# Kernel tuning notes

Hardware: AMD Instinct MI355X
Metric: run time of the kernel (lower is better)

Reference implementation:

```python
import jax, jax.numpy as jnp
import numpy as np

THETA_BASE = 10000.0

def rope(x, pos_offset=0):
    # x: (B, S, D), D even. Rotates interleaved (even, odd) dim pairs.
    B, S, D = x.shape
    pos = jnp.arange(pos_offset, pos_offset + S, dtype=jnp.float32)[:, None]  # (S,1)
    p = jnp.arange(D // 2, dtype=jnp.float32)  # p-1 in source, 0-indexed here
    theta = pos * (THETA_BASE ** (-2.0 * p / D))  # (S, D//2)
    sin_t, cos_t = jnp.sin(theta), jnp.cos(theta)
    x1, x2 = x[..., 0::2], x[..., 1::2]
    r1 = x1 * cos_t - x2 * sin_t
    r2 = x1 * sin_t + x2 * cos_t
    return jnp.stack((r1, r2), axis=-1).reshape(B, S, D)

def setup_inputs() -> dict:
    key = jax.random.key(0)
    k1, k2, k3, k4 = jax.random.split(key, 4)
    B, S, E, Dh = 4, 4096, 2048, 128
    return {
        "x": jax.random.normal(k1, (B, S, E), dtype=jnp.float32),
        "W_Q": jax.random.normal(k2, (E, Dh), dtype=jnp.float32) / np.sqrt(E),
        "W_K": jax.random.normal(k3, (E, Dh), dtype=jnp.float32) / np.sqrt(E),
        "W_V": jax.random.normal(k4, (E, Dh), dtype=jnp.float32) / np.sqrt(E),
    }

def reference(x, W_Q, W_K, W_V):
    d_h = W_Q.shape[1]
    past_len = 0  # kv_cache is None (prefill)
    Q = rope(x @ W_Q, pos_offset=past_len)  # NOTE: source ropes Q and V, not K
    K = x @ W_K
    V = rope(x @ W_V, pos_offset=past_len)
    scores = jnp.einsum('bqd,bkd->bqk', Q, K) / jnp.sqrt(jnp.float32(d_h))
    S_q, S_total = scores.shape[-2], scores.shape[-1]
    i = jnp.arange(S_q)[:, None] + past_len
    j = jnp.arange(S_total)[None, :]
    causal = j <= i  # (S_q, S_total) bool
    masked = jnp.where(causal[None, :, :], scores, jnp.float32(-jnp.inf))
    attn = jax.nn.softmax(masked, axis=-1)
    return jnp.einsum('bqk,bkd->bqd', attn, V)
```

## Files before the change

### kernel.cpp

```cpp
#include <hip/hip_runtime.h>
#include <hip/hip_bf16.h>
#include <stdint.h>

#define S_LEN 4096
#define E_DIM 2048
#define DH    128

typedef __bf16 bf16_t;
typedef bf16_t bf16x8 __attribute__((ext_vector_type(8)));
typedef float  f32x4  __attribute__((ext_vector_type(4)));

__device__ __forceinline__ unsigned short f2bf(float f) {
  union { float f; uint32_t u; } v; v.f = f;
  uint32_t u = v.u;
  uint32_t r = (u + 0x7fffu + ((u >> 16) & 1u)) >> 16;
  return (unsigned short)r;
}

__device__ __forceinline__ bf16x8 ld_bf16x8(const unsigned short* p) {
  return *(const bf16x8*)p;
}

__device__ __forceinline__ f32x4 mfma16(bf16x8 a, bf16x8 b, f32x4 c) {
  return __builtin_amdgcn_mfma_f32_16x16x32_bf16(a, b, c, 0, 0, 0);
}

__device__ __forceinline__ void gload16(const void* gsrc, void* ldst) {
  __builtin_amdgcn_global_load_lds(
      (const __attribute__((address_space(1))) uint32_t*)gsrc,
      (__attribute__((address_space(3))) uint32_t*)ldst, 16, 0, 0);
}

__global__ __launch_bounds__(256) void prep_kernel(
    const float* __restrict__ WQ, const float* __restrict__ WK,
    const float* __restrict__ WV,
    float2* __restrict__ trig, unsigned short* __restrict__ Wt)
{
  const int bx  = blockIdx.x;
  const int tid = threadIdx.x;
  if (bx < 1024) {
    const int idx = bx * 256 + tid;
    const int pos = idx >> 6, p = idx & 63;
    const float freq = powf(10000.0f, -(float)p / 64.0f);
    float sv, cv;
    sincosf((float)pos * freq, &sv, &cv);
    trig[idx] = make_float2(cv, sv);
    return;
  }
  __shared__ float lds[64][65];
  const int t   = bx - 1024;
  const int z   = t >> 6;
  const int rem = t & 63;
  const int k0  = (rem >> 1) * 64;
  const int n0  = (rem & 1) * 64;
  const float* W = (z == 0) ? WQ : ((z == 1) ? WK : WV);
  #pragma unroll
  for (int pass = 0; pass < 4; pass++) {
    const int r  = pass * 16 + (tid >> 4);
    const int c4 = (tid & 15) * 4;
    float4 v = *(const float4*)(W + (size_t)(k0 + r) * 128 + n0 + c4);
    lds[c4 + 0][r] = v.x; lds[c4 + 1][r] = v.y;
    lds[c4 + 2][r] = v.z; lds[c4 + 3][r] = v.w;
  }
  __syncthreads();
  #pragma unroll
  for (int pass = 0; pass < 4; pass++) {
    const int n  = pass * 16 + (tid >> 4);
    const int k4 = (tid & 15) * 4;
    ushort4 pk;
    pk.x = f2bf(lds[n][k4 + 0]); pk.y = f2bf(lds[n][k4 + 1]);
    pk.z = f2bf(lds[n][k4 + 2]); pk.w = f2bf(lds[n][k4 + 3]);
    *(ushort4*)(Wt + (size_t)(z * 128 + n0 + n) * E_DIM + k0 + k4) = pk;
  }
}

__global__ __launch_bounds__(256, 4) void proj_kernel(
    const float* __restrict__ x, const unsigned short* __restrict__ Wt,
    const float2* __restrict__ trig,
    unsigned short* __restrict__ Qb, unsigned short* __restrict__ Kb,
    unsigned short* __restrict__ Vt)
{
  __shared__ __align__(16) uint8_t Abuf[2][64 * 128];
  __shared__ __align__(16) uint8_t Bbuf[2][96 * 128];

  const int tid  = threadIdx.x;
  const int lane = tid & 63, w2 = tid >> 6;
  const int wr = w2 & 1, wc = w2 >> 1;
  const int col = lane & 15, kg = lane >> 4;

  const int m0 = blockIdx.x * 64;
  const int p  = blockIdx.y;

  f32x4 acc[2][3];
  #pragma unroll
  for (int i = 0; i < 2; i++)
    #pragma unroll
    for (int j = 0; j < 3; j++) acc[i][j] = (f32x4){0.f, 0.f, 0.f, 0.f};

  const int a_r = lane >> 4;
  const int a_c = (lane & 15) * 4;
  const int b_r  = lane >> 3;
  const int b_cb = (lane & 7) * 16;

  float4 R0[4], R1[4];

  #define ALOAD(R, K0)                                                        \
    do {                                                                      \
      _Pragma("unroll")                                                       \
      for (int j = 0; j < 4; j++) {                                           \
        const int row = w2 * 16 + j * 4 + a_r;                                \
        R[j] = *(const float4*)(x + (size_t)(m0 + row) * E_DIM + (K0) + a_c); \
      }                                                                       \
    } while (0)

  #define BSTAGE(K0, BUF)                                                     \
    do {                                                                      \
      _Pragma("unroll")                                                       \
      for (int c = 0; c < 3; c++) {                                           \
        const int seg = w2 * 3 + c;                                           \
        const int row = seg * 8 + b_r;                                        \
        const int src = b_cb ^ ((row & 7) << 4);                              \
        gload16((const char*)Wt + ((size_t)(p * 96 + row) * E_DIM + (K0)) * 2 + src,\
                &Bbuf[BUF][seg * 1024]);                                      \
      }                                                                       \
    } while (0)

  #define AWRITE(R, BUF)                                                      \
    do {                                                                      \
      _Pragma("unroll")                                                       \
      for (int j = 0; j < 4; j++) {                                           \
        const int row = w2 * 16 + j * 4 + a_r;                                \
        ushort4 h;                                                            \
        h.x = f2bf(R[j].x); h.y = f2bf(R[j].y);                               \
        h.z = f2bf(R[j].z); h.w = f2bf(R[j].w);                               \
        const int dst = (a_c * 2) ^ ((row & 7) << 4);                         \
        *(ushort4*)(&Abuf[BUF][row * 128 + dst]) = h;                         \
      }                                                                       \
    } while (0)

  #define COMP(BUF)                                                           \
    do {                                                                      \
      _Pragma("unroll")                                                       \
      for (int kk = 0; kk < 2; kk++) {                                        \
        bf16x8 af[2];                                                         \
        _Pragma("unroll")                                                     \
        for (int i = 0; i < 2; i++) {                                         \
          const int row = wr * 32 + i * 16 + col;                             \
          af[i] = *(const bf16x8*)(&Abuf[BUF][row * 128 +                     \
                   ((kk * 64 + kg * 16) ^ ((row & 7) << 4))]);                \
        }                                                                     \
        _Pragma("unroll")                                                     \
        for (int ns = 0; ns < 3; ns++) {                                      \
          const int n = wc * 48 + ns * 16 + col;                              \
          bf16x8 bf = *(const bf16x8*)(&Bbuf[BUF][n * 128 +                   \
                      ((kk * 64 + kg * 16) ^ ((n & 7) << 4))]);               \
          _Pragma("unroll")                                                   \
          for (int i = 0; i < 2; i++)                                         \
            acc[i][ns] = mfma16(af[i], bf, acc[i][ns]);                       \
        }                                                                     \
      }                                                                       \
    } while (0)

  BSTAGE(0, 0);
  __builtin_amdgcn_sched_barrier(0);
  ALOAD(R0, 0);
  ALOAD(R1, 64);
  __builtin_amdgcn_sched_barrier(0);
  AWRITE(R0, 0);
  asm volatile("s_waitcnt lgkmcnt(0)" ::: "memory");
  __builtin_amdgcn_sched_barrier(0);
  __builtin_amdgcn_s_barrier();

  #define BODY(I, RLD, RWR)                                                   \
    BSTAGE(((I) + 1) * 64, ((I) + 1) & 1);                                    \
    __builtin_amdgcn_sched_barrier(0);                                        \
    ALOAD(RLD, ((I) + 2) * 64);                                               \
    __builtin_amdgcn_sched_barrier(0);                                        \
    asm volatile("s_waitcnt vmcnt(11)" ::: "memory");                         \
    __builtin_amdgcn_sched_barrier(0);                                        \
    COMP((I) & 1);                                                            \
    AWRITE(RWR, ((I) + 1) & 1);                                               \
    asm volatile("s_waitcnt lgkmcnt(0)" ::: "memory");                        \
    __builtin_amdgcn_sched_barrier(0);                                        \
    __builtin_amdgcn_s_barrier();

  for (int ii = 0; ii < 15; ii++) {
    const int i0 = 2 * ii;
    BODY(i0, R0, R1)
    BODY(i0 + 1, R1, R0)
  }

  BSTAGE(31 * 64, 1);
  __builtin_amdgcn_sched_barrier(0);
  asm volatile("s_waitcnt vmcnt(7)" ::: "memory");
  __builtin_amdgcn_sched_barrier(0);
  COMP(0);
  AWRITE(R1, 1);
  asm volatile("s_waitcnt lgkmcnt(0)" ::: "memory");
  __builtin_amdgcn_sched_barrier(0);
  __builtin_amdgcn_s_barrier();

  asm volatile("s_waitcnt vmcnt(0)" ::: "memory");
  __builtin_amdgcn_sched_barrier(0);
  COMP(1);

  #undef BODY
  #undef ALOAD
  #undef BSTAGE
  #undef AWRITE
  #undef COMP

  #pragma unroll
  for (int i = 0; i < 2; i++) {
    const int mbase = m0 + wr * 32 + i * 16 + kg * 4;
    const int spos  = mbase & 4095;
    const int bb    = mbase >> 12;
    #pragma unroll
    for (int ns = 0; ns < 3; ns++) {
      const int n = p * 96 + wc * 48 + ns * 16 + col;
      const int z = n >> 7, d = n & 127;
      f32x4 v = acc[i][ns];
      if (z == 1) {
        #pragma unroll
        for (int r = 0; r < 4; r++)
          Kb[(size_t)(mbase + r) * DH + d] = f2bf(v[r]);
      } else {
        const float sgn  = (d & 1) ? 1.0f : -1.0f;
        const int   pidx = d >> 1;
        float ov[4];
        #pragma unroll
        for (int r = 0; r < 4; r++) {
          float  pv = __shfl_xor(v[r], 1, 64);
          float2 cs = trig[(spos + r) * 64 + pidx];
          ov[r] = v[r] * cs.x + sgn * pv * cs.y;
        }
        if (z == 0) {
          #pragma unroll
          for (int r = 0; r < 4; r++)
            Qb[(size_t)(mbase + r) * DH + d] =
                f2bf(ov[r] * 0.08838834764831845f);
        } else {
          ushort4 pk;
          pk.x = f2bf(ov[0]); pk.y = f2bf(ov[1]);
          pk.z = f2bf(ov[2]); pk.w = f2bf(ov[3]);
          *(ushort4*)(Vt + ((size_t)(bb * DH + d)) * S_LEN + spos) = pk;
        }
      }
    }
  }
}

__global__ __launch_bounds__(256, 2) void flash_kernel(
    const unsigned short* __restrict__ Qb, const unsigned short* __restrict__ Kb,
    const unsigned short* __restrict__ Vt, float* __restrict__ out)
{
  __shared__ __align__(16) unsigned short Ktile[128 * 128];
  __shared__ __align__(16) unsigned short Vtile[128 * 128];
  __shared__ __align__(16) unsigned short Plds[4][16][72];

  const int bid  = blockIdx.x;
  const int half = bid >> 8, rb = bid & 255;
  const int qi   = half ? (127 - (rb >> 1)) : (rb >> 1);
  const int b    = (rb & 1) | (half << 1);
  const int q0   = qi * 32;

  const int tid = threadIdx.x;
  const int lane = tid & 63, w = tid >> 6;
  const int h   = w & 1;
  const int kvh = w >> 1;
  const int col = lane & 15, kg = lane >> 4;

  bf16x8 qf[4];
  {
    const unsigned short* qrow =
        Qb + (size_t)(b * S_LEN + q0 + h * 16 + col) * DH;
    #pragma unroll
    for (int kk = 0; kk < 4; kk++)
      qf[kk] = ld_bf16x8(qrow + kk * 32 + kg * 8);
  }

  f32x4 o[8];
  #pragma unroll
  for (int i = 0; i < 8; i++) o[i] = (f32x4){0.f, 0.f, 0.f, 0.f};
  float mrow[4] = {-1e30f, -1e30f, -1e30f, -1e30f};
  float lrow[4] = {0.f, 0.f, 0.f, 0.f};

  const char* Kbase = (const char*)(Kb + (size_t)b * S_LEN * DH);
  const char* Vbase = (const char*)(Vt + (size_t)b * DH * S_LEN);

  const int r_off = lane >> 4, colb = (lane & 15) * 16;

  for (int kv0 = 0; kv0 < q0 + 32; kv0 += 128) {
    #pragma unroll
    for (int c = 0; c < 8; c++) {
      const int row = w * 32 + c * 4 + r_off;
      const int src = colb ^ ((row & 7) << 4);
      gload16(Kbase + (size_t)(kv0 + row) * 256 + src,
              (char*)Ktile + w * 8192 + c * 1024);
    }
    #pragma unroll
    for (int c = 0; c < 8; c++) {
      const int d   = w * 32 + c * 4 + r_off;
      const int src = colb ^ ((d & 7) << 4);
      gload16(Vbase + (size_t)d * 8192 + (size_t)kv0 * 2 + src,
              (char*)Vtile + w * 8192 + c * 1024);
    }
    __syncthreads();

    f32x4 st[4];
    __builtin_amdgcn_s_setprio(1);
    #pragma unroll
    for (int kb = 0; kb < 4; kb++) {
      f32x4 sacc = (f32x4){0.f, 0.f, 0.f, 0.f};
      const int krow = kvh * 64 + kb * 16 + col;
      #pragma unroll
      for (int kk = 0; kk < 4; kk++) {
        bf16x8 kf = *(const bf16x8*)((const char*)Ktile + krow * 256 +
                                     ((kk * 64 + kg * 16) ^ ((krow & 7) << 4)));
        sacc = mfma16(qf[kk], kf, sacc);
      }
      st[kb] = sacc;
    }
    __builtin_amdgcn_s_setprio(0);

    if (kv0 + 127 > q0) {
      #pragma unroll
      for (int kb = 0; kb < 4; kb++) {
        const int key = kv0 + kvh * 64 + kb * 16 + col;
        #pragma unroll
        for (int r = 0; r < 4; r++) {
          const int q = q0 + h * 16 + kg * 4 + r;
          if (key > q) st[kb][r] = -1e30f;
        }
      }
    }

    float scale[4];
    #pragma unroll
    for (int r = 0; r < 4; r++) {
      float mx = fmaxf(fmaxf(st[0][r], st[1][r]), fmaxf(st[2][r], st[3][r]));
      #pragma unroll
      for (int off = 1; off < 16; off <<= 1)
        mx = fmaxf(mx, __shfl_xor(mx, off, 64));
      const float mnew = fmaxf(mrow[r], mx);
      scale[r] = __expf(mrow[r] - mnew);
      mrow[r] = mnew;
      float psum = 0.f;
      #pragma unroll
      for (int kb = 0; kb < 4; kb++) {
        float pexp = __expf(st[kb][r] - mnew);
        st[kb][r] = pexp;
        psum += pexp;
      }
      lrow[r] = lrow[r] * scale[r] + psum;
    }
    #pragma unroll
    for (int nt = 0; nt < 8; nt++)
      #pragma unroll
      for (int r = 0; r < 4; r++)
        o[nt][r] *= scale[r];

    #pragma unroll
    for (int kb = 0; kb < 4; kb++)
      #pragma unroll
      for (int r = 0; r < 4; r++)
        Plds[w][kg * 4 + r][kb * 16 + col] = f2bf(st[kb][r]);

    __builtin_amdgcn_s_setprio(1);
    #pragma unroll
    for (int kc = 0; kc < 2; kc++) {
      bf16x8 pa = ld_bf16x8(&Plds[w][col][kc * 32 + kg * 8]);
      #pragma unroll
      for (int nt = 0; nt < 8; nt++) {
        const int vrow = nt * 16 + col;
        bf16x8 vf = *(const bf16x8*)((const char*)Vtile + vrow * 256 +
            ((kvh * 128 + kc * 64 + kg * 16) ^ ((vrow & 7) << 4)));
        o[nt] = mfma16(pa, vf, o[nt]);
      }
    }
    __builtin_amdgcn_s_setprio(0);
    __syncthreads();
  }

  float lfull[4];
  #pragma unroll
  for (int r = 0; r < 4; r++) {
    float l = lrow[r];
    #pragma unroll
    for (int off = 1; off < 16; off <<= 1)
      l += __shfl_xor(l, off, 64);
    lfull[r] = l;
  }

  float* Olds = (float*)Ktile;
  float* Ml   = (float*)Vtile;
  #pragma unroll
  for (int nt = 0; nt < 8; nt++)
    #pragma unroll
    for (int r = 0; r < 4; r++)
      Olds[(w * 16 + kg * 4 + r) * 128 + nt * 16 + col] = o[nt][r];
  if (col == 0) {
    #pragma unroll
    for (int r = 0; r < 4; r++) {
      Ml[w * 16 + kg * 4 + r]      = mrow[r];
      Ml[64 + w * 16 + kg * 4 + r] = lfull[r];
    }
  }
  __syncthreads();
  if (w < 2) {
    #pragma unroll
    for (int r = 0; r < 4; r++) {
      const int row = kg * 4 + r;
      const float m1 = Ml[w * 16 + row],        l1 = Ml[64 + w * 16 + row];
      const float m2 = Ml[(w + 2) * 16 + row],  l2 = Ml[64 + (w + 2) * 16 + row];
      const float mf = fmaxf(m1, m2);
      const float w1 = __expf(m1 - mf), wgt2 = __expf(m2 - mf);
      const float inv = 1.0f / (l1 * w1 + l2 * wgt2);
      float* orow = out + (size_t)(b * S_LEN + q0 + w * 16 + row) * DH;
      #pragma unroll
      for (int nt = 0; nt < 8; nt++) {
        const float v1 = Olds[(w * 16 + row) * 128 + nt * 16 + col];
        const float v2 = Olds[((w + 2) * 16 + row) * 128 + nt * 16 + col];
        orow[nt * 16 + col] = (v1 * w1 + v2 * wgt2) * inv;
      }
    }
  }
}

extern "C" void kernel_launch(void* const* d_in, const int* in_sizes, int n_in,
                              void* d_out, int out_size, void* d_ws, size_t ws_size,
                              hipStream_t stream) {
  const float* x  = (const float*)d_in[0];
  const float* WQ = (const float*)d_in[1];
  const float* WK = (const float*)d_in[2];
  const float* WV = (const float*)d_in[3];
  float* out = (float*)d_out;

  char* ws = (char*)d_ws;
  float2*         trig = (float2*)(ws);
  unsigned short* Wt   = (unsigned short*)(ws + (2u << 20));
  unsigned short* Qb   = (unsigned short*)(ws + (4u << 20));
  unsigned short* Kb   = (unsigned short*)(ws + (8u << 20));
  unsigned short* Vt   = (unsigned short*)(ws + (12u << 20));

  hipLaunchKernelGGL(prep_kernel, dim3(1216), dim3(256), 0, stream,
                     WQ, WK, WV, trig, Wt);
  hipLaunchKernelGGL(proj_kernel, dim3(256, 4), dim3(256), 0, stream,
                     x, Wt, trig, Qb, Kb, Vt);
  hipLaunchKernelGGL(flash_kernel, dim3(512), dim3(256), 0, stream,
                     Qb, Kb, Vt, out);
}
```

Baseline: 147.8 us.

## Double-buffer 64-key K/V tiles to overlap global loads with MFMA compute

Replaces the single 128-key K/V LDS tile with two 64-key buffers and prefetches the next tile while computing on the current one, using vmcnt waits and raw barriers. Smaller tiles also trim the causal tail work for diagonal blocks. The aim is to hide global-load latency that previously stalled behind __syncthreads, at the cost of twice as many iterations, more barriers and shorter MFMA bursts per iteration.

Result: slower. 174.8 us (+18.2%).

```diff
diff --git a/kernel.cpp b/kernel.cpp
--- a/kernel.cpp
+++ b/kernel.cpp
@@ -254,9 +254,9 @@
     const unsigned short* __restrict__ Qb, const unsigned short* __restrict__ Kb,
     const unsigned short* __restrict__ Vt, float* __restrict__ out)
 {
-  __shared__ __align__(16) unsigned short Ktile[128 * 128];
-  __shared__ __align__(16) unsigned short Vtile[128 * 128];
-  __shared__ __align__(16) unsigned short Plds[4][16][72];
+  __shared__ __align__(16) unsigned short Ktile[2][64 * 128];
+  __shared__ __align__(16) unsigned short Vtile[2][128 * 64];
+  __shared__ __align__(16) unsigned short Plds[4][16][40];
 
   const int bid  = blockIdx.x;
   const int half = bid >> 8, rb = bid & 255;
@@ -267,7 +267,7 @@
   const int tid = threadIdx.x;
   const int lane = tid & 63, w = tid >> 6;
   const int h   = w & 1;
-  const int kvh = w >> 1;
+  const int kvq = w >> 1;
   const int col = lane & 15, kg = lane >> 4;
 
   bf16x8 qf[4];
@@ -288,34 +288,56 @@
   const char* Kbase = (const char*)(Kb + (size_t)b * S_LEN * DH);
   const char* Vbase = (const char*)(Vt + (size_t)b * DH * S_LEN);
 
-  const int r_off = lane >> 4, colb = (lane & 15) * 16;
-
-  for (int kv0 = 0; kv0 < q0 + 32; kv0 += 128) {
-    #pragma unroll
-    for (int c = 0; c < 8; c++) {
-      const int row = w * 32 + c * 4 + r_off;
-      const int src = colb ^ ((row & 7) << 4);
-      gload16(Kbase + (size_t)(kv0 + row) * 256 + src,
-              (char*)Ktile + w * 8192 + c * 1024);
-    }
-    #pragma unroll
-    for (int c = 0; c < 8; c++) {
-      const int d   = w * 32 + c * 4 + r_off;
-      const int src = colb ^ ((d & 7) << 4);
-      gload16(Vbase + (size_t)d * 8192 + (size_t)kv0 * 2 + src,
-              (char*)Vtile + w * 8192 + c * 1024);
-    }
-    __syncthreads();
-
-    f32x4 st[4];
+  const int kr  = lane >> 4;
+  const int kcb = (lane & 15) * 16;
+  const int vr  = lane >> 3;
+  const int vcb = (lane & 7) * 16;
+
+  #define STAGE(T, BUF)                                                       \
+    do {                                                                      \
+      const int kv0s = (T) * 64;                                              \
+      _Pragma("unroll")                                                       \
+      for (int c = 0; c < 4; c++) {                                           \
+        const int row = w * 16 + c * 4 + kr;                                  \
+        const int src = kcb ^ ((row & 7) << 4);                               \
+        gload16(Kbase + (size_t)(kv0s + row) * 256 + src,                     \
+                (char*)Ktile[BUF] + (w * 16 + c * 4) * 256);                  \
+      }                                                                       \
+      _Pragma("unroll")                                                       \
+      for (int c = 0; c < 4; c++) {                                           \
+        const int dD  = w * 32 + c * 8 + vr;                                  \
+        const int src = vcb ^ ((dD & 7) << 4);                                \
+        gload16(Vbase + (size_t)dD * 8192 + (size_t)kv0s * 2 + src,           \
+                (char*)Vtile[BUF] + (w * 32 + c * 8) * 128);                  \
+      }                                                                       \
+    } while (0)
+
+  const int T = (q0 + 95) >> 6;
+
+  STAGE(0, 0);
+
+  for (int t = 0; t < T; t++) {
+    if (t + 1 < T) {
+      STAGE(t + 1, (t + 1) & 1);
+      asm volatile("s_waitcnt vmcnt(8)" ::: "memory");
+    } else {
+      asm volatile("s_waitcnt vmcnt(0)" ::: "memory");
+    }
+    __builtin_amdgcn_sched_barrier(0);
+    __builtin_amdgcn_s_barrier();
+
+    const int buf = t & 1;
+    const int kv0 = t * 64;
+
+    f32x4 st[2];
     __builtin_amdgcn_s_setprio(1);
     #pragma unroll
-    for (int kb = 0; kb < 4; kb++) {
+    for (int kb = 0; kb < 2; kb++) {
       f32x4 sacc = (f32x4){0.f, 0.f, 0.f, 0.f};
-      const int krow = kvh * 64 + kb * 16 + col;
+      const int krow = kvq * 32 + kb * 16 + col;
       #pragma unroll
       for (int kk = 0; kk < 4; kk++) {
-        bf16x8 kf = *(const bf16x8*)((const char*)Ktile + krow * 256 +
+        bf16x8 kf = *(const bf16x8*)((const char*)Ktile[buf] + krow * 256 +
                                      ((kk * 64 + kg * 16) ^ ((krow & 7) << 4)));
         sacc = mfma16(qf[kk], kf, sacc);
       }
@@ -323,10 +345,10 @@
     }
     __builtin_amdgcn_s_setprio(0);
 
-    if (kv0 + 127 > q0) {
-      #pragma unroll
-      for (int kb = 0; kb < 4; kb++) {
-        const int key = kv0 + kvh * 64 + kb * 16 + col;
+    if (kv0 + 63 > q0) {
+      #pragma unroll
+      for (int kb = 0; kb < 2; kb++) {
+        const int key = kv0 + kvq * 32 + kb * 16 + col;
         #pragma unroll
         for (int r = 0; r < 4; r++) {
           const int q = q0 + h * 16 + kg * 4 + r;
@@ -338,7 +360,7 @@
     float scale[4];
     #pragma unroll
     for (int r = 0; r < 4; r++) {
-      float mx = fmaxf(fmaxf(st[0][r], st[1][r]), fmaxf(st[2][r], st[3][r]));
+      float mx = fmaxf(st[0][r], st[1][r]);
       #pragma unroll
       for (int off = 1; off < 16; off <<= 1)
         mx = fmaxf(mx, __shfl_xor(mx, off, 64));
@@ -347,7 +369,7 @@
       mrow[r] = mnew;
       float psum = 0.f;
       #pragma unroll
-      for (int kb = 0; kb < 4; kb++) {
+      for (int kb = 0; kb < 2; kb++) {
         float pexp = __expf(st[kb][r] - mnew);
         st[kb][r] = pexp;
         psum += pexp;
@@ -361,26 +383,26 @@
         o[nt][r] *= scale[r];
 
     #pragma unroll
-    for (int kb = 0; kb < 4; kb++)
+    for (int kb = 0; kb < 2; kb++)
       #pragma unroll
       for (int r = 0; r < 4; r++)
         Plds[w][kg * 4 + r][kb * 16 + col] = f2bf(st[kb][r]);
 
     __builtin_amdgcn_s_setprio(1);
-    #pragma unroll
-    for (int kc = 0; kc < 2; kc++) {
-      bf16x8 pa = ld_bf16x8(&Plds[w][col][kc * 32 + kg * 8]);
+    {
+      bf16x8 pa = ld_bf16x8(&Plds[w][col][kg * 8]);
       #pragma unroll
       for (int nt = 0; nt < 8; nt++) {
         const int vrow = nt * 16 + col;
-        bf16x8 vf = *(const bf16x8*)((const char*)Vtile + vrow * 256 +
-            ((kvh * 128 + kc * 64 + kg * 16) ^ ((vrow & 7) << 4)));
+        bf16x8 vf = *(const bf16x8*)((const char*)Vtile[buf] + vrow * 128 +
+            ((kvq * 64 + kg * 16) ^ ((vrow & 7) << 4)));
         o[nt] = mfma16(pa, vf, o[nt]);
       }
     }
     __builtin_amdgcn_s_setprio(0);
-    __syncthreads();
-  }
+    __builtin_amdgcn_s_barrier();
+  }
+  #undef STAGE
 
   float lfull[4];
   #pragma unroll
```
